# Kernel optimization log

Hardware: AMD Instinct MI355X
Metric: run time of the kernel (lower is better)

## Reference

```python
import jax, jax.numpy as jnp
import numpy as np

EPS = 1e-8
SOFTEN = 1.0
COLOR_NORM = 1.0


def setup_inputs() -> dict:
    key = jax.random.key(0)
    k1, k2, k3, k4 = jax.random.split(key, 4)
    B, C, H, W = 16, 3, 224, 224
    K, HID = 64, 256
    img = jax.random.uniform(k1, (B, C, H, W), dtype=jnp.float32)
    W1 = jax.random.normal(k2, (HID, C), dtype=jnp.float32) * 0.1
    b1 = jax.random.normal(k3, (HID,), dtype=jnp.float32) * 0.1
    W2 = jax.random.normal(k4, (K, HID), dtype=jnp.float32) * 0.1
    return {"img": img, "W1": W1, "b1": b1, "W2": W2}


def reference(img, W1, b1, W2):
    # color_mask: 1x1 conv (3->256) + ReLU + 1x1 conv (256->K, no bias)
    h = jax.nn.relu(jnp.einsum('bchw,oc->bohw', img, W1) + b1[None, :, None, None])
    logits = jnp.einsum('bohw,ko->bkhw', h, W2)
    # Softmax2d == softmax over channel dim; soften=1
    m = jax.nn.softmax(SOFTEN * logits, axis=1)  # (B,K,H,W)
    # training=True path: soft weighted palette.
    # (img[:,:,None]*m[:,None]).sum(spatial) contracted directly via einsum
    # to avoid materializing the (B,3,K,H,W) broadcast tensor.
    num = jnp.einsum('bchw,bkhw->bck', img, m)          # (B,3,K)
    den = jnp.sum(m, axis=(2, 3))                        # (B,K)
    palette = num / (den[:, None, :] + EPS) / COLOR_NORM  # (B,3,K)
    # color_jitter=0 -> jitter_palette == palette
    transformed_img = jnp.einsum('bkhw,bck->bchw', m, palette)
    # match torch shape (B,3,K,1,1) for palette output
    return transformed_img, m, palette[:, :, :, None, None]
```

## Files before the change

### kernel.cpp

```cpp
#include <hip/hip_runtime.h>
#include <hip/hip_bf16.h>

#define BATCH 16
#define HW 50176
#define HID 256
#define K 64

#define OUT_T_OFF 0
#define OUT_M_OFF 2408448
#define OUT_P_OFF 53788672

#define WS_DEN 0
#define WS_NUM 1024
#define WS_W1P 4096
#define WS_W2B 5120

typedef short bf16x8 __attribute__((ext_vector_type(8)));
typedef float f32x4  __attribute__((ext_vector_type(4)));

static __device__ __forceinline__ short f2bf(float x) {
    union { __hip_bfloat16 h; short s; } u;
    u.h = __float2bfloat16(x);
    return u.s;
}

__global__ __launch_bounds__(256) void colorcnn_prep(
    const float* __restrict__ W1, const float* __restrict__ b1,
    const float* __restrict__ W2, float* __restrict__ wsf,
    float4* __restrict__ w1p, ushort* __restrict__ w2b)
{
    const int t = threadIdx.x;
    if (blockIdx.x == 0) {
#pragma unroll
        for (int q = 0; q < 16; ++q) wsf[q * 256 + t] = 0.f;
        w1p[t] = make_float4(W1[3 * t], W1[3 * t + 1], W1[3 * t + 2], b1[t]);
    }
#pragma unroll
    for (int q = 0; q < 8; ++q) {
        const int i = (blockIdx.x * 8 + q) * 256 + t;
        w2b[i] = (ushort)f2bf(W2[i]);
    }
}

__global__ __launch_bounds__(256, 4) void colorcnn_mlp_softmax(
    const float* __restrict__ img, const float4* __restrict__ w1p,
    const ushort* __restrict__ w2b, float* __restrict__ m_out,
    float* __restrict__ den_ws, float* __restrict__ num_ws)
{
    __shared__ int4 lds[2304];
    __shared__ float sred[4][256];

    const int t = threadIdx.x;
    const int4* w2b16 = (const int4*)w2b;
#pragma unroll
    for (int q = 0; q < 8; ++q) {
        const int i = t + q * 256;
        const int n = i >> 5, s = i & 31;
        lds[n * 32 + (s ^ (n & 7))] = w2b16[i];
    }
    lds[2048 + t] = ((const int4*)w1p)[t];
    __syncthreads();

    const int b    = blockIdx.y;
    const int pb   = blockIdx.x * 128;
    const int w    = t >> 6;
    const int lane = t & 63;
    const int l15  = lane & 15;
    const int lg   = lane >> 4;
    const int pwb  = pb + w * 32;
    const int x7   = l15 & 7;

    const float* ip = img + (size_t)b * 3 * HW;

    float rr[2], gg[2], uu[2];
#pragma unroll
    for (int s = 0; s < 2; ++s) {
        const int px = pwb + s * 16 + l15;
        rr[s] = ip[px]; gg[s] = ip[HW + px]; uu[s] = ip[2 * HW + px];
    }

    f32x4 acc[2][4];
#pragma unroll
    for (int s = 0; s < 2; ++s)
#pragma unroll
        for (int ni = 0; ni < 4; ++ni)
            acc[s][ni] = (f32x4){0.f, 0.f, 0.f, 0.f};

    const float4* w1l = (const float4*)&lds[2048 + lg * 8];

#pragma unroll
    for (int c = 0; c < 8; ++c) {
        union { bf16x8 v; unsigned int u[4]; } ua0, ua1;
#pragma unroll
        for (int p = 0; p < 4; ++p) {
            const float4 wv0 = w1l[c * 32 + 2 * p];
            const float4 wv1 = w1l[c * 32 + 2 * p + 1];
            const float e0 = fmaxf(fmaf(rr[0], wv0.x, fmaf(gg[0], wv0.y, fmaf(uu[0], wv0.z, wv0.w))), 0.f);
            const float o0 = fmaxf(fmaf(rr[0], wv1.x, fmaf(gg[0], wv1.y, fmaf(uu[0], wv1.z, wv1.w))), 0.f);
            const float e1 = fmaxf(fmaf(rr[1], wv0.x, fmaf(gg[1], wv0.y, fmaf(uu[1], wv0.z, wv0.w))), 0.f);
            const float o1 = fmaxf(fmaf(rr[1], wv1.x, fmaf(gg[1], wv1.y, fmaf(uu[1], wv1.z, wv1.w))), 0.f);
            __hip_bfloat162 c0 = __float22bfloat162_rn(float2{e0, o0});
            __hip_bfloat162 c1 = __float22bfloat162_rn(float2{e1, o1});
            ua0.u[p] = *(unsigned int*)&c0;
            ua1.u[p] = *(unsigned int*)&c1;
        }
        const int sw = (c * 4 + lg) ^ x7;
#pragma unroll
        for (int ni = 0; ni < 4; ++ni) {
            const bf16x8 bf = *(const bf16x8*)&lds[(ni * 16 + l15) * 32 + sw];
            acc[0][ni] = __builtin_amdgcn_mfma_f32_16x16x32_bf16(ua0.v, bf, acc[0][ni], 0, 0, 0);
            acc[1][ni] = __builtin_amdgcn_mfma_f32_16x16x32_bf16(ua1.v, bf, acc[1][ni], 0, 0, 0);
        }
    }

#pragma unroll
    for (int s = 0; s < 2; ++s) {
#pragma unroll
        for (int reg = 0; reg < 4; ++reg) {
            const float v0 = __expf(acc[s][0][reg]);
            const float v1 = __expf(acc[s][1][reg]);
            const float v2 = __expf(acc[s][2][reg]);
            const float v3 = __expf(acc[s][3][reg]);
            float sm = (v0 + v1) + (v2 + v3);
            sm += __shfl_xor(sm, 1);
            sm += __shfl_xor(sm, 2);
            sm += __shfl_xor(sm, 4);
            sm += __shfl_xor(sm, 8);
            const float inv = __builtin_amdgcn_rcpf(sm);
            acc[s][0][reg] = v0 * inv; acc[s][1][reg] = v1 * inv;
            acc[s][2][reg] = v2 * inv; acc[s][3][reg] = v3 * inv;
        }
    }

    float red[16];
#pragma unroll
    for (int i = 0; i < 16; ++i) red[i] = 0.f;
#pragma unroll
    for (int s = 0; s < 2; ++s) {
        const int pxb = pwb + s * 16 + lg * 4;
        const f32x4 rC = *(const f32x4*)&ip[pxb];
        const f32x4 gC = *(const f32x4*)&ip[HW + pxb];
        const f32x4 uC = *(const f32x4*)&ip[2 * HW + pxb];
#pragma unroll
        for (int ni = 0; ni < 4; ++ni) {
#pragma unroll
            for (int reg = 0; reg < 4; ++reg) {
                const float mv = acc[s][ni][reg];
                red[ni]      += mv;
                red[4 + ni]   = fmaf(rC[reg], mv, red[4 + ni]);
                red[8 + ni]   = fmaf(gC[reg], mv, red[8 + ni]);
                red[12 + ni]  = fmaf(uC[reg], mv, red[12 + ni]);
            }
        }
    }
#pragma unroll
    for (int i = 0; i < 16; ++i) {
        red[i] += __shfl_xor(red[i], 16);
        red[i] += __shfl_xor(red[i], 32);
    }
    if (lg == 0) {
#pragma unroll
        for (int ni = 0; ni < 4; ++ni) {
            const int n = ni * 16 + l15;
            sred[w][n]       = red[ni];
            sred[w][64 + n]  = red[4 + ni];
            sred[w][128 + n] = red[8 + ni];
            sred[w][192 + n] = red[12 + ni];
        }
    }
    __syncthreads();
    {
        const int q = t >> 6, n = t & 63;
        const float v = sred[0][t] + sred[1][t] + sred[2][t] + sred[3][t];
        if (q == 0) atomicAdd(&den_ws[b * K + n], v);
        else        atomicAdd(&num_ws[(b * 3 + (q - 1)) * K + n], v);
    }

    float* mo = m_out + (size_t)b * K * HW + pwb;
#pragma unroll
    for (int s = 0; s < 2; ++s)
#pragma unroll
        for (int ni = 0; ni < 4; ++ni) {
            const int n = ni * 16 + l15;
            *(f32x4*)&mo[(size_t)n * HW + s * 16 + lg * 4] = acc[s][ni];
        }
}

__global__ __launch_bounds__(256) void colorcnn_reconstruct(
    const float* __restrict__ m, const float* __restrict__ den_ws,
    const float* __restrict__ num_ws, float* __restrict__ pal_out,
    float* __restrict__ t_out)
{
    __shared__ float pl[192];
    const int b    = blockIdx.x / 49;
    const int tile = blockIdx.x % 49;
    const int t    = threadIdx.x;

    if (t < 192) {
        const int c = t >> 6, k = t & 63;
        const float v = num_ws[(b * 3 + c) * K + k] / (den_ws[b * K + k] + 1e-8f);
        pl[t] = v;
        if (tile == 0) pal_out[b * 3 * K + t] = v;
    }
    __syncthreads();

    const int p = tile * 1024 + t * 4;
    const float* mp = m + (size_t)b * K * HW + p;
    f32x4 ar = {0.f, 0.f, 0.f, 0.f}, ag = ar, ab = ar;
#pragma unroll
    for (int k = 0; k < K; ++k) {
        const f32x4 mv = *(const f32x4*)&mp[(size_t)k * HW];
        const float pr = pl[k], pg = pl[K + k], pu = pl[2 * K + k];
#pragma unroll
        for (int j = 0; j < 4; ++j) {
            ar[j] = fmaf(mv[j], pr, ar[j]);
            ag[j] = fmaf(mv[j], pg, ag[j]);
            ab[j] = fmaf(mv[j], pu, ab[j]);
        }
    }
    float* to = t_out + (size_t)b * 3 * HW + p;
    *(f32x4*)&to[0]      = ar;
    *(f32x4*)&to[HW]     = ag;
    *(f32x4*)&to[2 * HW] = ab;
}

extern "C" void kernel_launch(void* const* d_in, const int* in_sizes, int n_in,
                              void* d_out, int out_size, void* d_ws, size_t ws_size,
                              hipStream_t stream) {
    const float* img = (const float*)d_in[0];
    const float* W1  = (const float*)d_in[1];
    const float* b1  = (const float*)d_in[2];
    const float* W2  = (const float*)d_in[3];

    float* out   = (float*)d_out;
    float* t_out = out + OUT_T_OFF;
    float* m_out = out + OUT_M_OFF;
    float* p_out = out + OUT_P_OFF;

    float*  wsf    = (float*)d_ws;
    float*  den_ws = wsf + WS_DEN;
    float*  num_ws = wsf + WS_NUM;
    float4* w1p    = (float4*)(wsf + WS_W1P);
    ushort* w2b    = (ushort*)(wsf + WS_W2B);

    colorcnn_prep<<<8, 256, 0, stream>>>(W1, b1, W2, wsf, w1p, w2b);
    colorcnn_mlp_softmax<<<dim3(HW / 128, BATCH), 256, 0, stream>>>(img, w1p, w2b, m_out, den_ws, num_ws);
    colorcnn_reconstruct<<<BATCH * 49, 256, 0, stream>>>(m_out, den_ws, num_ws, p_out, t_out);
}
```

Baseline: 125.0 us.

## Drop block-level LDS reduction for per-wave atomics, halve reconstruct tile size

The MLP/softmax kernel now writes the mask m before doing the palette reductions. It also replaces the LDS cross-wave reduction and __syncthreads with direct per-wave atomicAdds, spread across lane groups so each group handles den or one colour channel. This removes a block barrier and LDS traffic, at the cost of four times more global atomics to a small set of addresses. The reconstruct kernel uses a 2D grid with 512-pixel tiles and float2 loads, doubling block count to 98x16 for more parallelism, with narrower memory accesses.

```diff
diff --git a/kernel.cpp b/kernel.cpp
--- a/kernel.cpp
+++ b/kernel.cpp
@@ -17,6 +17,7 @@
 
 typedef short bf16x8 __attribute__((ext_vector_type(8)));
 typedef float f32x4  __attribute__((ext_vector_type(4)));
+typedef float f32x2  __attribute__((ext_vector_type(2)));
 
 static __device__ __forceinline__ short f2bf(float x) {
     union { __hip_bfloat16 h; short s; } u;
@@ -48,7 +49,6 @@
     float* __restrict__ den_ws, float* __restrict__ num_ws)
 {
     __shared__ int4 lds[2304];
-    __shared__ float sred[4][256];
 
     const int t = threadIdx.x;
     const int4* w2b16 = (const int4*)w2b;
@@ -132,6 +132,15 @@
         }
     }
 
+    float* mo = m_out + (size_t)b * K * HW + pwb;
+#pragma unroll
+    for (int s = 0; s < 2; ++s)
+#pragma unroll
+        for (int ni = 0; ni < 4; ++ni) {
+            const int n = ni * 16 + l15;
+            *(f32x4*)&mo[(size_t)n * HW + s * 16 + lg * 4] = acc[s][ni];
+        }
+
     float red[16];
 #pragma unroll
     for (int i = 0; i < 16; ++i) red[i] = 0.f;
@@ -158,32 +167,31 @@
         red[i] += __shfl_xor(red[i], 16);
         red[i] += __shfl_xor(red[i], 32);
     }
-    if (lg == 0) {
-#pragma unroll
-        for (int ni = 0; ni < 4; ++ni) {
-            const int n = ni * 16 + l15;
-            sred[w][n]       = red[ni];
-            sred[w][64 + n]  = red[4 + ni];
-            sred[w][128 + n] = red[8 + ni];
-            sred[w][192 + n] = red[12 + ni];
-        }
-    }
-    __syncthreads();
     {
-        const int q = t >> 6, n = t & 63;
-        const float v = sred[0][t] + sred[1][t] + sred[2][t] + sred[3][t];
-        if (q == 0) atomicAdd(&den_ws[b * K + n], v);
-        else        atomicAdd(&num_ws[(b * 3 + (q - 1)) * K + n], v);
-    }
-
-    float* mo = m_out + (size_t)b * K * HW + pwb;
-#pragma unroll
-    for (int s = 0; s < 2; ++s)
-#pragma unroll
-        for (int ni = 0; ni < 4; ++ni) {
-            const int n = ni * 16 + l15;
-            *(f32x4*)&mo[(size_t)n * HW + s * 16 + lg * 4] = acc[s][ni];
-        }
+        float* db = den_ws + b * K;
+        float* nb = num_ws + b * 3 * K;
+        if (lg == 0) {
+            atomicAdd(&db[l15],      red[0]);
+            atomicAdd(&db[16 + l15], red[1]);
+            atomicAdd(&db[32 + l15], red[2]);
+            atomicAdd(&db[48 + l15], red[3]);
+        } else if (lg == 1) {
+            atomicAdd(&nb[l15],      red[4]);
+            atomicAdd(&nb[16 + l15], red[5]);
+            atomicAdd(&nb[32 + l15], red[6]);
+            atomicAdd(&nb[48 + l15], red[7]);
+        } else if (lg == 2) {
+            atomicAdd(&nb[K + l15],      red[8]);
+            atomicAdd(&nb[K + 16 + l15], red[9]);
+            atomicAdd(&nb[K + 32 + l15], red[10]);
+            atomicAdd(&nb[K + 48 + l15], red[11]);
+        } else {
+            atomicAdd(&nb[2 * K + l15],      red[12]);
+            atomicAdd(&nb[2 * K + 16 + l15], red[13]);
+            atomicAdd(&nb[2 * K + 32 + l15], red[14]);
+            atomicAdd(&nb[2 * K + 48 + l15], red[15]);
+        }
+    }
 }
 
 __global__ __launch_bounds__(256) void colorcnn_reconstruct(
@@ -192,8 +200,8 @@
     float* __restrict__ t_out)
 {
     __shared__ float pl[192];
-    const int b    = blockIdx.x / 49;
-    const int tile = blockIdx.x % 49;
+    const int b    = blockIdx.y;
+    const int tile = blockIdx.x;
     const int t    = threadIdx.x;
 
     if (t < 192) {
@@ -204,24 +212,24 @@
     }
     __syncthreads();
 
-    const int p = tile * 1024 + t * 4;
+    const int p = tile * 512 + t * 2;
     const float* mp = m + (size_t)b * K * HW + p;
-    f32x4 ar = {0.f, 0.f, 0.f, 0.f}, ag = ar, ab = ar;
+    f32x2 ar = {0.f, 0.f}, ag = ar, ab = ar;
 #pragma unroll
     for (int k = 0; k < K; ++k) {
-        const f32x4 mv = *(const f32x4*)&mp[(size_t)k * HW];
+        const f32x2 mv = *(const f32x2*)&mp[(size_t)k * HW];
         const float pr = pl[k], pg = pl[K + k], pu = pl[2 * K + k];
 #pragma unroll
-        for (int j = 0; j < 4; ++j) {
+        for (int j = 0; j < 2; ++j) {
             ar[j] = fmaf(mv[j], pr, ar[j]);
             ag[j] = fmaf(mv[j], pg, ag[j]);
             ab[j] = fmaf(mv[j], pu, ab[j]);
         }
     }
     float* to = t_out + (size_t)b * 3 * HW + p;
-    *(f32x4*)&to[0]      = ar;
-    *(f32x4*)&to[HW]     = ag;
-    *(f32x4*)&to[2 * HW] = ab;
+    *(f32x2*)&to[0]      = ar;
+    *(f32x2*)&to[HW]     = ag;
+    *(f32x2*)&to[2 * HW] = ab;
 }
 
 extern "C" void kernel_launch(void* const* d_in, const int* in_sizes, int n_in,
@@ -245,5 +253,5 @@
 
     colorcnn_prep<<<8, 256, 0, stream>>>(W1, b1, W2, wsf, w1p, w2b);
     colorcnn_mlp_softmax<<<dim3(HW / 128, BATCH), 256, 0, stream>>>(img, w1p, w2b, m_out, den_ws, num_ws);
-    colorcnn_reconstruct<<<BATCH * 49, 256, 0, stream>>>(m_out, den_ws, num_ws, p_out, t_out);
-}
+    colorcnn_reconstruct<<<dim3(HW / 512, BATCH), 256, 0, stream>>>(m_out, den_ws, num_ws, p_out, t_out);
+}
```

After: 211.8 us. +69.4%, slower.

## Stream W2 in double-buffered LDS chunks with 512-thread blocks

Applied to the files above, without the earlier changes.

The prep kernel now pre-swizzles bf16 W2 into four HID chunks. The main kernel keeps only two 8KB chunk buffers in LDS instead of the full 32KB matrix and prefetches the next chunk into registers while computing the current one. Blocks grow to 512 threads (8 waves, 256 pixels), and the W1 table gets an XOR swizzle. The aim is to cut LDS footprint and per-block weight staging cost so more blocks fit per CU, at the price of three extra block barriers inside the K loop.

```diff
diff --git a/kernel.cpp b/kernel.cpp
--- a/kernel.cpp
+++ b/kernel.cpp
@@ -18,8 +18,8 @@
 typedef short bf16x8 __attribute__((ext_vector_type(8)));
 typedef float f32x4  __attribute__((ext_vector_type(4)));
 
-static __device__ __forceinline__ short f2bf(float x) {
-    union { __hip_bfloat16 h; short s; } u;
+static __device__ __forceinline__ ushort f2bf(float x) {
+    union { __hip_bfloat16 h; ushort s; } u;
     u.h = __float2bfloat16(x);
     return u.s;
 }
@@ -27,7 +27,7 @@
 __global__ __launch_bounds__(256) void colorcnn_prep(
     const float* __restrict__ W1, const float* __restrict__ b1,
     const float* __restrict__ W2, float* __restrict__ wsf,
-    float4* __restrict__ w1p, ushort* __restrict__ w2b)
+    float4* __restrict__ w1p, int4* __restrict__ w2b4)
 {
     const int t = threadIdx.x;
     if (blockIdx.x == 0) {
@@ -35,34 +35,35 @@
         for (int q = 0; q < 16; ++q) wsf[q * 256 + t] = 0.f;
         w1p[t] = make_float4(W1[3 * t], W1[3 * t + 1], W1[3 * t + 2], b1[t]);
     }
-#pragma unroll
-    for (int q = 0; q < 8; ++q) {
-        const int i = (blockIdx.x * 8 + q) * 256 + t;
-        w2b[i] = (ushort)f2bf(W2[i]);
-    }
-}
-
-__global__ __launch_bounds__(256, 4) void colorcnn_mlp_softmax(
-    const float* __restrict__ img, const float4* __restrict__ w1p,
-    const ushort* __restrict__ w2b, float* __restrict__ m_out,
+    const int g  = blockIdx.x * 256 + t;
+    const int ch = g >> 9;
+    const int n  = (g >> 3) & 63;
+    const int jj = g & 7;
+    const int cl = jj >> 2;
+    const int lg = jj & 3;
+    const int hid0 = ch * 64 + cl * 32 + lg * 8;
+    union { int4 v; ushort u[8]; } un;
+#pragma unroll
+    for (int e = 0; e < 8; ++e) un.u[e] = f2bf(W2[n * HID + hid0 + e]);
+    w2b4[ch * 512 + n * 8 + (jj ^ (n & 7))] = un.v;
+}
+
+__global__ __launch_bounds__(512, 8) void colorcnn_mlp_softmax(
+    const float* __restrict__ img, const int4* __restrict__ w1p4,
+    const int4* __restrict__ w2b4, float* __restrict__ m_out,
     float* __restrict__ den_ws, float* __restrict__ num_ws)
 {
-    __shared__ int4 lds[2304];
-    __shared__ float sred[4][256];
+    __shared__ int4  wbuf[2][512];
+    __shared__ int4  w1l[256];
+    __shared__ float sred[8][256];
 
     const int t = threadIdx.x;
-    const int4* w2b16 = (const int4*)w2b;
-#pragma unroll
-    for (int q = 0; q < 8; ++q) {
-        const int i = t + q * 256;
-        const int n = i >> 5, s = i & 31;
-        lds[n * 32 + (s ^ (n & 7))] = w2b16[i];
-    }
-    lds[2048 + t] = ((const int4*)w1p)[t];
+    wbuf[0][t] = w2b4[t];
+    if (t < 256) w1l[t ^ ((t >> 3) & 3)] = w1p4[t];
     __syncthreads();
 
     const int b    = blockIdx.y;
-    const int pb   = blockIdx.x * 128;
+    const int pb   = blockIdx.x * 256;
     const int w    = t >> 6;
     const int lane = t & 63;
     const int l15  = lane & 15;
@@ -86,30 +87,39 @@
         for (int ni = 0; ni < 4; ++ni)
             acc[s][ni] = (f32x4){0.f, 0.f, 0.f, 0.f};
 
-    const float4* w1l = (const float4*)&lds[2048 + lg * 8];
-
-#pragma unroll
-    for (int c = 0; c < 8; ++c) {
-        union { bf16x8 v; unsigned int u[4]; } ua0, ua1;
-#pragma unroll
-        for (int p = 0; p < 4; ++p) {
-            const float4 wv0 = w1l[c * 32 + 2 * p];
-            const float4 wv1 = w1l[c * 32 + 2 * p + 1];
-            const float e0 = fmaxf(fmaf(rr[0], wv0.x, fmaf(gg[0], wv0.y, fmaf(uu[0], wv0.z, wv0.w))), 0.f);
-            const float o0 = fmaxf(fmaf(rr[0], wv1.x, fmaf(gg[0], wv1.y, fmaf(uu[0], wv1.z, wv1.w))), 0.f);
-            const float e1 = fmaxf(fmaf(rr[1], wv0.x, fmaf(gg[1], wv0.y, fmaf(uu[1], wv0.z, wv0.w))), 0.f);
-            const float o1 = fmaxf(fmaf(rr[1], wv1.x, fmaf(gg[1], wv1.y, fmaf(uu[1], wv1.z, wv1.w))), 0.f);
-            __hip_bfloat162 c0 = __float22bfloat162_rn(float2{e0, o0});
-            __hip_bfloat162 c1 = __float22bfloat162_rn(float2{e1, o1});
-            ua0.u[p] = *(unsigned int*)&c0;
-            ua1.u[p] = *(unsigned int*)&c1;
-        }
-        const int sw = (c * 4 + lg) ^ x7;
-#pragma unroll
-        for (int ni = 0; ni < 4; ++ni) {
-            const bf16x8 bf = *(const bf16x8*)&lds[(ni * 16 + l15) * 32 + sw];
-            acc[0][ni] = __builtin_amdgcn_mfma_f32_16x16x32_bf16(ua0.v, bf, acc[0][ni], 0, 0, 0);
-            acc[1][ni] = __builtin_amdgcn_mfma_f32_16x16x32_bf16(ua1.v, bf, acc[1][ni], 0, 0, 0);
+#pragma unroll
+    for (int ch = 0; ch < 4; ++ch) {
+        int4 stg;
+        if (ch < 3) stg = w2b4[(ch + 1) * 512 + t];
+#pragma unroll
+        for (int cl = 0; cl < 2; ++cl) {
+            const int c = ch * 2 + cl;
+            union { bf16x8 v; unsigned int u[4]; } ua0, ua1;
+#pragma unroll
+            for (int p = 0; p < 4; ++p) {
+                const int hid0 = c * 32 + lg * 8 + 2 * p;
+                const float4 wv0 = *(const float4*)&w1l[hid0 ^ lg];
+                const float4 wv1 = *(const float4*)&w1l[(hid0 + 1) ^ lg];
+                const float e0 = fmaxf(fmaf(rr[0], wv0.x, fmaf(gg[0], wv0.y, fmaf(uu[0], wv0.z, wv0.w))), 0.f);
+                const float o0 = fmaxf(fmaf(rr[0], wv1.x, fmaf(gg[0], wv1.y, fmaf(uu[0], wv1.z, wv1.w))), 0.f);
+                const float e1 = fmaxf(fmaf(rr[1], wv0.x, fmaf(gg[1], wv0.y, fmaf(uu[1], wv0.z, wv0.w))), 0.f);
+                const float o1 = fmaxf(fmaf(rr[1], wv1.x, fmaf(gg[1], wv1.y, fmaf(uu[1], wv1.z, wv1.w))), 0.f);
+                __hip_bfloat162 c0 = __float22bfloat162_rn(float2{e0, o0});
+                __hip_bfloat162 c1 = __float22bfloat162_rn(float2{e1, o1});
+                ua0.u[p] = *(unsigned int*)&c0;
+                ua1.u[p] = *(unsigned int*)&c1;
+            }
+            const int sw = (cl * 4 + lg) ^ x7;
+#pragma unroll
+            for (int ni = 0; ni < 4; ++ni) {
+                const bf16x8 bf = *(const bf16x8*)&wbuf[ch & 1][(ni * 16 + l15) * 8 + sw];
+                acc[0][ni] = __builtin_amdgcn_mfma_f32_16x16x32_bf16(ua0.v, bf, acc[0][ni], 0, 0, 0);
+                acc[1][ni] = __builtin_amdgcn_mfma_f32_16x16x32_bf16(ua1.v, bf, acc[1][ni], 0, 0, 0);
+            }
+        }
+        if (ch < 3) {
+            wbuf[(ch + 1) & 1][t] = stg;
+            __syncthreads();
         }
     }
 
@@ -169,9 +179,11 @@
         }
     }
     __syncthreads();
-    {
+    if (t < 256) {
         const int q = t >> 6, n = t & 63;
-        const float v = sred[0][t] + sred[1][t] + sred[2][t] + sred[3][t];
+        float v = sred[0][t];
+#pragma unroll
+        for (int wv = 1; wv < 8; ++wv) v += sred[wv][t];
         if (q == 0) atomicAdd(&den_ws[b * K + n], v);
         else        atomicAdd(&num_ws[(b * 3 + (q - 1)) * K + n], v);
     }
@@ -241,9 +253,9 @@
     float*  den_ws = wsf + WS_DEN;
     float*  num_ws = wsf + WS_NUM;
     float4* w1p    = (float4*)(wsf + WS_W1P);
-    ushort* w2b    = (ushort*)(wsf + WS_W2B);
-
-    colorcnn_prep<<<8, 256, 0, stream>>>(W1, b1, W2, wsf, w1p, w2b);
-    colorcnn_mlp_softmax<<<dim3(HW / 128, BATCH), 256, 0, stream>>>(img, w1p, w2b, m_out, den_ws, num_ws);
+    int4*   w2b4   = (int4*)(wsf + WS_W2B);
+
+    colorcnn_prep<<<8, 256, 0, stream>>>(W1, b1, W2, wsf, w1p, w2b4);
+    colorcnn_mlp_softmax<<<dim3(HW / 256, BATCH), 512, 0, stream>>>(img, (const int4*)w1p, w2b4, m_out, den_ws, num_ws);
     colorcnn_reconstruct<<<BATCH * 49, 256, 0, stream>>>(m_out, den_ws, num_ws, p_out, t_out);
 }
```

New measurement: 176.6 us. 1.41x slower.
